# Kernel tuning notes

Hardware: AMD Instinct MI355X
Metric: run time of the kernel (lower is better)

The kernel has to match this reference:

```python
import jax, jax.numpy as jnp
import numpy as np

B, S, D, H = 4, 2048, 1024, 16
HD = D // H


def setup_inputs() -> dict:
    key = jax.random.key(0)
    ks = jax.random.split(key, 5)
    s_in = 1.0 / np.sqrt(D)
    return {
        "x": jax.random.normal(ks[0], (B, S, D), dtype=jnp.float32),
        "W_attn": jax.random.uniform(ks[1], (D, 3 * D), dtype=jnp.float32, minval=-s_in, maxval=s_in),
        "b_attn": jax.random.uniform(ks[2], (3 * D,), dtype=jnp.float32, minval=-s_in, maxval=s_in),
        "W_proj": jax.random.uniform(ks[3], (D, D), dtype=jnp.float32, minval=-s_in, maxval=s_in),
        "b_proj": jax.random.uniform(ks[4], (D,), dtype=jnp.float32, minval=-s_in, maxval=s_in),
    }


def reference(x, W_attn, b_attn, W_proj, b_proj):
    b, s, d = x.shape
    qkv = x @ W_attn + b_attn                      # [B,S,3D]
    q, k, v = jnp.split(qkv, 3, axis=-1)
    # [B,H,S,HD]
    q = q.reshape(b, s, H, HD).transpose(0, 2, 1, 3)
    k = k.reshape(b, s, H, HD).transpose(0, 2, 1, 3)
    v = v.reshape(b, s, H, HD).transpose(0, 2, 1, 3)
    scale = 1.0 / np.sqrt(HD)
    att = jnp.einsum("bhqd,bhkd->bhqk", q, k) * scale
    causal = jnp.tril(jnp.ones((s, s), dtype=bool))
    att = jnp.where(causal[None, None], att, -jnp.inf)
    att = jax.nn.softmax(att, axis=-1)
    y = jnp.einsum("bhqk,bhkd->bhqd", att, v)      # [B,H,S,HD]
    y = y.transpose(0, 2, 1, 3).reshape(b, s, d)
    return y @ W_proj + b_proj
```

## Files before the change

### kernel.cpp

```cpp
#include <hip/hip_runtime.h>

#define B_  4
#define S_  2048
#define D_  1024
#define H_  16
#define HD_ 64
#define BS_ (B_*S_)

typedef _Float16 f16;
typedef _Float16 f16_8 __attribute__((ext_vector_type(8)));
typedef _Float16 f16_4 __attribute__((ext_vector_type(4)));
typedef float    f32_4 __attribute__((ext_vector_type(4)));
typedef unsigned int u32;

#define MFMA32(a,b,c) __builtin_amdgcn_mfma_f32_16x16x32_f16(a, b, c, 0, 0, 0)
#define MFMA16(a,b,c) __builtin_amdgcn_mfma_f32_16x16x16f16(a, b, c, 0, 0, 0)
#define NEG_INF (-__builtin_inff())

__device__ inline void gl_lds16(const f16* g, f16* lds_base, int chunk_base) {
    __builtin_amdgcn_global_load_lds(
        (const __attribute__((address_space(1))) u32*)g,
        (__attribute__((address_space(3))) u32*)(lds_base + (size_t)chunk_base * 8),
        16, 0, 0);
}

__global__ __launch_bounds__(256) void prep(
    const float* __restrict__ X,  f16* __restrict__ Xh,
    const float* __restrict__ Wa, f16* __restrict__ Wta)
{
    __shared__ f16 T[64][72];
    const int t = threadIdx.x;
    const int bid = blockIdx.x;
    if (bid < 4096) {
        const size_t i = ((size_t)bid * 256 + t) * 8;
        float4 a = *(const float4*)&X[i];
        float4 b = *(const float4*)&X[i + 4];
        f16 h[8] = {(f16)a.x,(f16)a.y,(f16)a.z,(f16)a.w,
                    (f16)b.x,(f16)b.y,(f16)b.z,(f16)b.w};
        *(uint4*)&Xh[i] = *(const uint4*)h;
        return;
    }
    const int idx = bid - 4096;
    const int n0 = (idx % 48) * 64, k0 = (idx / 48) * 64;
    const int nl4 = (t & 15) * 4;
    #pragma unroll
    for (int r = 0; r < 4; r++) {
        const int kl = (t >> 4) + r * 16;
        float4 v = *(const float4*)&Wa[(size_t)(k0 + kl) * 3072 + n0 + nl4];
        T[nl4 + 0][kl] = (f16)v.x;
        T[nl4 + 1][kl] = (f16)v.y;
        T[nl4 + 2][kl] = (f16)v.z;
        T[nl4 + 3][kl] = (f16)v.w;
    }
    __syncthreads();
    const int nr = t >> 2, kc = (t & 3) * 16;
    *(uint4*)&Wta[(size_t)(n0 + nr) * 1024 + k0 + kc]     = *(uint4*)&T[nr][kc];
    *(uint4*)&Wta[(size_t)(n0 + nr) * 1024 + k0 + kc + 8] = *(uint4*)&T[nr][kc + 8];
}

__global__ __launch_bounds__(256) void trans_w(
    const float* __restrict__ W, f16* __restrict__ Wt, int ncols)
{
    __shared__ f16 T[64][72];
    const int t = threadIdx.x;
    const int n0 = blockIdx.x * 64, k0 = blockIdx.y * 64;
    const int nl4 = (t & 15) * 4;
    #pragma unroll
    for (int r = 0; r < 4; r++) {
        const int kl = (t >> 4) + r * 16;
        float4 v = *(const float4*)&W[(size_t)(k0 + kl) * ncols + n0 + nl4];
        T[nl4 + 0][kl] = (f16)v.x;
        T[nl4 + 1][kl] = (f16)v.y;
        T[nl4 + 2][kl] = (f16)v.z;
        T[nl4 + 3][kl] = (f16)v.w;
    }
    __syncthreads();
    const int nr = t >> 2, kc = (t & 3) * 16;
    *(uint4*)&Wt[(size_t)(n0 + nr) * 1024 + k0 + kc]     = *(uint4*)&T[nr][kc];
    *(uint4*)&Wt[(size_t)(n0 + nr) * 1024 + k0 + kc + 8] = *(uint4*)&T[nr][kc + 8];
}

__global__ __launch_bounds__(512, 2) void qkv_gemm(
    const f16*   __restrict__ Xh,
    const f16*   __restrict__ Wta,
    const float* __restrict__ bias,
    f16* __restrict__ Qb, f16* __restrict__ Kb, f16* __restrict__ Vt)
{
    __shared__ f16 lds[73728];

    const int t    = threadIdx.x;
    const int lane = t & 63;
    const int w    = t >> 6;
    const int quad = lane >> 4, l15 = lane & 15;
    const int wr = w >> 2, wc = w & 3;
    const int m0 = blockIdx.x * 128;
    const int n0 = blockIdx.y * 256;
    const int wb = t & 448;

    int aoff[2], boff[4];
    #pragma unroll
    for (int c = 0; c < 2; c++) {
        const int i = c*512 + t, row = i >> 3, sl = i & 7;
        aoff[c] = row*1024 + ((sl ^ (row & 7)) << 3);
    }
    #pragma unroll
    for (int c = 0; c < 4; c++) {
        const int i = c*512 + t, row = i >> 3, sl = i & 7;
        boff[c] = row*1024 + ((sl ^ (row & 7)) << 3);
    }
    int fa[4][2], fb[4][2];
    #pragma unroll
    for (int mi = 0; mi < 4; mi++)
        #pragma unroll
        for (int kk = 0; kk < 2; kk++)
            fa[mi][kk] = (wr*64 + mi*16 + l15)*64 + (((kk*4 + quad) ^ (l15 & 7)) << 3);
    #pragma unroll
    for (int ni = 0; ni < 4; ni++)
        #pragma unroll
        for (int kk = 0; kk < 2; kk++)
            fb[ni][kk] = (wc*64 + ni*16 + l15)*64 + (((kk*4 + quad) ^ (l15 & 7)) << 3);

    const f16* Ag = Xh  + (size_t)m0 * 1024;
    const f16* Bg = Wta + (size_t)n0 * 1024;

    f32_4 acc[4][4] = {};

    #pragma unroll
    for (int c = 0; c < 2; c++) gl_lds16(Ag + aoff[c],       lds,                c*512 + wb);
    #pragma unroll
    for (int c = 0; c < 4; c++) gl_lds16(Bg + boff[c],       lds + 8192,         c*512 + wb);
    #pragma unroll
    for (int c = 0; c < 2; c++) gl_lds16(Ag + 64 + aoff[c],  lds + 24576,        c*512 + wb);
    #pragma unroll
    for (int c = 0; c < 4; c++) gl_lds16(Bg + 64 + boff[c],  lds + 24576 + 8192, c*512 + wb);
    asm volatile("s_waitcnt vmcnt(6)" ::: "memory");
    __builtin_amdgcn_s_barrier();
    asm volatile("" ::: "memory");

    int cur = 0;
    #pragma unroll 1
    for (int T = 0; T < 16; T++) {
        f16* buf        = lds + cur*24576;
        const int nxt   = cur ? cur - 1 : 2;
        f16* nbuf       = lds + nxt*24576;
        const bool st   = (T < 14);
        const int  kt2  = (T + 2) * 64;

        if (st) {
            #pragma unroll
            for (int c = 0; c < 2; c++)
                gl_lds16(Ag + kt2 + aoff[c], nbuf, c*512 + wb);
        }
        f16_8 af[4][2], bf[2][2];
        #pragma unroll
        for (int mi = 0; mi < 4; mi++)
            #pragma unroll
            for (int kk = 0; kk < 2; kk++)
                af[mi][kk] = *(const f16_8*)&buf[fa[mi][kk]];
        #pragma unroll
        for (int ni = 0; ni < 2; ni++)
            #pragma unroll
            for (int kk = 0; kk < 2; kk++)
                bf[ni][kk] = *(const f16_8*)&buf[8192 + fb[ni][kk]];
        asm volatile("" ::: "memory");
        __builtin_amdgcn_s_barrier();
        asm volatile("" ::: "memory");
        __builtin_amdgcn_s_setprio(1);
        #pragma unroll
        for (int kk = 0; kk < 2; kk++)
            #pragma unroll
            for (int mi = 0; mi < 4; mi++)
                #pragma unroll
                for (int ni = 0; ni < 2; ni++)
                    acc[mi][ni] = MFMA32(af[mi][kk], bf[ni][kk], acc[mi][ni]);
        __builtin_amdgcn_s_setprio(0);
        asm volatile("" ::: "memory");
        __builtin_amdgcn_s_barrier();
        asm volatile("" ::: "memory");

        if (st) {
            #pragma unroll
            for (int c = 0; c < 4; c++)
                gl_lds16(Bg + kt2 + boff[c], nbuf + 8192, c*512 + wb);
        }
        #pragma unroll
        for (int ni = 0; ni < 2; ni++)
            #pragma unroll
            for (int kk = 0; kk < 2; kk++)
                bf[ni][kk] = *(const f16_8*)&buf[8192 + fb[2 + ni][kk]];
        asm volatile("" ::: "memory");
        __builtin_amdgcn_s_barrier();
        asm volatile("" ::: "memory");
        __builtin_amdgcn_s_setprio(1);
        #pragma unroll
        for (int kk = 0; kk < 2; kk++)
            #pragma unroll
            for (int mi = 0; mi < 4; mi++)
                #pragma unroll
                for (int ni = 0; ni < 2; ni++)
                    acc[mi][2 + ni] = MFMA32(af[mi][kk], bf[ni][kk], acc[mi][2 + ni]);
        __builtin_amdgcn_s_setprio(0);
        if (T < 14)       asm volatile("s_waitcnt vmcnt(6)" ::: "memory");
        else if (T == 14) asm volatile("s_waitcnt vmcnt(0)" ::: "memory");
        __builtin_amdgcn_s_barrier();
        asm volatile("" ::: "memory");

        cur = (cur >= 2) ? 0 : cur + 1;
    }

    const int which = n0 >> 10;
    float bcol[4];
    #pragma unroll
    for (int ni = 0; ni < 4; ni++)
        bcol[ni] = bias[n0 + wc*64 + ni*16 + l15];

    if (which < 2) {
        f16* dst = (which == 0) ? Qb : Kb;
        const float sc = (which == 0) ? 0.125f * 1.44269504f : 1.0f;
        #pragma unroll
        for (int mi = 0; mi < 4; mi++)
        #pragma unroll
        for (int ni = 0; ni < 4; ni++)
        #pragma unroll
        for (int r = 0; r < 4; r++) {
            int m = m0 + wr*64 + mi*16 + quad*4 + r;
            int n = (n0 & 1023) + wc*64 + ni*16 + l15;
            int h = n >> 6, hd = n & 63;
            int b = m >> 11, s = m & 2047;
            dst[((size_t)(b*16 + h)*2048 + s)*64 + hd] =
                (f16)((acc[mi][ni][r] + bcol[ni]) * sc);
        }
    } else {
        f16* Ct = lds;
        #pragma unroll
        for (int mi = 0; mi < 4; mi++)
        #pragma unroll
        for (int ni = 0; ni < 4; ni++)
        #pragma unroll
        for (int r = 0; r < 4; r++) {
            int nl = wc*64 + ni*16 + l15;
            int ml = wr*64 + mi*16 + quad*4 + r;
            Ct[nl*136 + ml] = (f16)(acc[mi][ni][r] + bcol[ni]);
        }
        __syncthreads();
        const int row = t >> 1, half = t & 1;
        const int nv = (n0 & 1023) + row;
        const int h = nv >> 6, hd = nv & 63;
        const int b = m0 >> 11;
        const int s0 = (m0 & 2047) + half*64;
        f16* dst = Vt + ((size_t)(b*16 + h)*64 + hd)*2048 + s0;
        #pragma unroll
        for (int j = 0; j < 8; j++)
            *(uint4*)&dst[j*8] = *(uint4*)&Ct[row*136 + half*64 + j*8];
    }
}

__global__ __launch_bounds__(256) void attn(
    const f16* __restrict__ Qb,
    const f16* __restrict__ Kb,
    const f16* __restrict__ Vt,
    f16* __restrict__ Y)
{
    __shared__ f16 Ks[64*72];
    __shared__ f16 Vs[64*72];

    const int t    = threadIdx.x;
    const int w    = t >> 6;
    const int lane = t & 63;
    const int quad = lane >> 4, l15 = lane & 15;
    const int bh   = blockIdx.x;
    const int b    = bh >> 4, h = bh & 15;

    const f16* qh = Qb + (size_t)bh * S_ * 64;
    const f16* kh = Kb + (size_t)bh * S_ * 64;
    const f16* vt = Vt + (size_t)bh * 64 * S_;

    const int sk = t >> 2, sc = (t & 3) * 8;
    const f16_4 ones = {(f16)1,(f16)1,(f16)1,(f16)1};

    #pragma unroll 1
    for (int sp = 0; sp < 2; sp++) {
        const int qb = sp ? 15 - (int)blockIdx.y : (int)blockIdx.y;
        const int qw = qb*128 + w*32;

        f16_8 qa[2][2];
        #pragma unroll
        for (int rt = 0; rt < 2; rt++)
            #pragma unroll
            for (int c = 0; c < 2; c++)
                qa[rt][c] = *(const f16_8*)&qh[(size_t)(qw + rt*16 + l15)*64 + c*32 + quad*8];

        f32_4 o[2][4] = {};
        f32_4 lacc[2] = {};
        const int ntiles = 2*qb + 2;

        for (int kt = 0; kt < ntiles; kt++) {
            const int kbase = kt * 64;
            *(uint4*)&Ks[sk*72 + sc]      = *(const uint4*)&kh[(size_t)(kbase + sk)*64 + sc];
            *(uint4*)&Ks[sk*72 + sc + 32] = *(const uint4*)&kh[(size_t)(kbase + sk)*64 + sc + 32];
            *(uint4*)&Vs[sk*72 + sc]      = *(const uint4*)&vt[(size_t)sk*2048 + kbase + sc];
            *(uint4*)&Vs[sk*72 + sc + 32] = *(const uint4*)&vt[(size_t)sk*2048 + kbase + sc + 32];
            __syncthreads();

            if (kbase <= qw + 31) {
                f16_8 kb[4][2];
                #pragma unroll
                for (int sub = 0; sub < 4; sub++)
                    #pragma unroll
                    for (int c = 0; c < 2; c++)
                        kb[sub][c] = *(const f16_8*)&Ks[(sub*16 + l15)*72 + c*32 + quad*8];
                f32_4 st[2][4];
                #pragma unroll
                for (int rt = 0; rt < 2; rt++)
                    #pragma unroll
                    for (int sub = 0; sub < 4; sub++) {
                        f32_4 a = {};
                        a = MFMA32(kb[sub][0], qa[rt][0], a);
                        a = MFMA32(kb[sub][1], qa[rt][1], a);
                        st[rt][sub] = a;
                    }

                const bool masked = (kbase + 63 > qw);
                f16_4 pt[2][4];
                #pragma unroll
                for (int rt = 0; rt < 2; rt++)
                #pragma unroll
                for (int sub = 0; sub < 4; sub++) {
                    const int qrow = qw + rt*16 + l15;
                    f16_4 p;
                    #pragma unroll
                    for (int r = 0; r < 4; r++) {
                        float x = st[rt][sub][r];
                        if (masked) {
                            int key = kbase + sub*16 + quad*4 + r;
                            x = (key <= qrow) ? x : NEG_INF;
                        }
                        p[r] = (f16)__builtin_amdgcn_exp2f(x);
                    }
                    pt[rt][sub] = p;
                }

                #pragma unroll
                for (int rt = 0; rt < 2; rt++) {
                    f16_4 ps = (pt[rt][0] + pt[rt][1]) + (pt[rt][2] + pt[rt][3]);
                    lacc[rt] = MFMA16(ps, ones, lacc[rt]);
                }

                #pragma unroll
                for (int sub = 0; sub < 4; sub++) {
                    f16_4 vb[4];
                    #pragma unroll
                    for (int tt = 0; tt < 4; tt++)
                        vb[tt] = *(const f16_4*)&Vs[(tt*16 + l15)*72 + sub*16 + quad*4];
                    #pragma unroll
                    for (int rt = 0; rt < 2; rt++)
                        #pragma unroll
                        for (int tt = 0; tt < 4; tt++)
                            o[rt][tt] = MFMA16(pt[rt][sub], vb[tt], o[rt][tt]);
                }
            }
            __syncthreads();
        }

        #pragma unroll
        for (int rt = 0; rt < 2; rt++)
        #pragma unroll
        for (int r = 0; r < 4; r++) {
            float inv = 1.0f / lacc[rt][r];
            int srow = qw + rt*16 + quad*4 + r;
            #pragma unroll
            for (int tt = 0; tt < 4; tt++)
                Y[(size_t)(b*S_ + srow)*1024 + h*64 + tt*16 + l15] =
                    (f16)(o[rt][tt][r] * inv);
        }
    }
}

__global__ __launch_bounds__(256) void proj_gemm(
    const f16* __restrict__ Yb,
    const f16* __restrict__ Wtp,
    const float* __restrict__ bias,
    float* __restrict__ Out)
{
    __shared__ f16 lds2[16384];
    f16* Af[2] = {lds2,        lds2 + 4096};
    f16* Bf[2] = {lds2 + 8192, lds2 + 12288};

    const int t    = threadIdx.x;
    const int lane = t & 63;
    const int w    = t >> 6;
    const int quad = lane >> 4, l15 = lane & 15;
    const int wr = w >> 1, wc = w & 1;
    const int m0 = blockIdx.x * 128;
    const int n0 = blockIdx.y * 128;
    const int wbase = t & 192;

    f32_4 acc[4][4] = {};

    for (int k0 = 0; k0 < 1024; k0 += 64) {
        #pragma unroll
        for (int kc = 0; kc < 2; kc++)
            #pragma unroll
            for (int c = 0; c < 2; c++) {
                int i = c*256 + t;
                const int row = i >> 2, col = (i & 3) * 8;
                gl_lds16(Yb  + (size_t)(m0 + row)*1024 + k0 + kc*32 + col,
                         Af[kc], c*256 + wbase);
                gl_lds16(Wtp + (size_t)(n0 + row)*1024 + k0 + kc*32 + col,
                         Bf[kc], c*256 + wbase);
            }
        __syncthreads();
        #pragma unroll
        for (int kc = 0; kc < 2; kc++) {
            f16_8 af[4], bf[4];
            #pragma unroll
            for (int mi = 0; mi < 4; mi++)
                af[mi] = *(const f16_8*)&Af[kc][(wr*64 + mi*16 + l15)*32 + quad*8];
            #pragma unroll
            for (int ni = 0; ni < 4; ni++)
                bf[ni] = *(const f16_8*)&Bf[kc][(wc*64 + ni*16 + l15)*32 + quad*8];
            #pragma unroll
            for (int mi = 0; mi < 4; mi++)
                #pragma unroll
                for (int ni = 0; ni < 4; ni++)
                    acc[mi][ni] = MFMA32(af[mi], bf[ni], acc[mi][ni]);
        }
        __syncthreads();
    }

    #pragma unroll
    for (int mi = 0; mi < 4; mi++)
    #pragma unroll
    for (int ni = 0; ni < 4; ni++)
    #pragma unroll
    for (int r = 0; r < 4; r++) {
        int m = m0 + wr*64 + mi*16 + quad*4 + r;
        int n = n0 + wc*64 + ni*16 + l15;
        Out[(size_t)m*1024 + n] = acc[mi][ni][r] + bias[n];
    }
}

extern "C" void kernel_launch(void* const* d_in, const int* in_sizes, int n_in,
                              void* d_out, int out_size, void* d_ws, size_t ws_size,
                              hipStream_t stream) {
    const float* x      = (const float*)d_in[0];
    const float* W_attn = (const float*)d_in[1];
    const float* b_attn = (const float*)d_in[2];
    const float* W_proj = (const float*)d_in[3];
    const float* b_proj = (const float*)d_in[4];
    float* out = (float*)d_out;

    const size_t per = (size_t)B_ * H_ * S_ * HD_;
    f16* Yb  = (f16*)d_ws;
    f16* Wta = Yb;
    f16* Qb  = Yb + per;
    f16* Kb  = Qb + per;
    f16* Vt  = Kb + per;
    f16* Wtp = Qb;
    f16* Xh  = (f16*)d_out;

    prep     <<<4096 + 768, 256, 0, stream>>>(x, Xh, W_attn, Wta);
    qkv_gemm <<<dim3(64, 12), 512, 0, stream>>>(Xh, Wta, b_attn, Qb, Kb, Vt);
    attn     <<<dim3(64, 8),  256, 0, stream>>>(Qb, Kb, Vt, Yb);
    trans_w  <<<dim3(16, 16), 256, 0, stream>>>(W_proj, Wtp, D_);
    proj_gemm<<<dim3(64, 8),  256, 0, stream>>>(Yb, Wtp, b_proj, out);
}
```

Baseline: 273.5 us.

## Restructure attention to 512 threads with double-buffered async K/V loads

The attention kernel now runs both paired query strips in one pass using 8 waves (512 threads) instead of looping over them sequentially. K/V tiles are loaded with global_load_lds into double-buffered, XOR-swizzled LDS, so the next tile's load overlaps compute on the current one, and raw s_barrier/waitcnt replace __syncthreads. MFMA sections get raised scheduling priority. This removes serialized load-then-compute stalls and LDS bank conflicts, at the cost of more LDS per block (64KB) and tighter register limits from launch_bounds(512,4).

```diff
diff --git a/kernel.cpp b/kernel.cpp
--- a/kernel.cpp
+++ b/kernel.cpp
@@ -255,14 +255,13 @@
     }
 }
 
-__global__ __launch_bounds__(256) void attn(
+__global__ __launch_bounds__(512, 4) void attn(
     const f16* __restrict__ Qb,
     const f16* __restrict__ Kb,
     const f16* __restrict__ Vt,
     f16* __restrict__ Y)
 {
-    __shared__ f16 Ks[64*72];
-    __shared__ f16 Vs[64*72];
+    __shared__ f16 lds[32768];
 
     const int t    = threadIdx.x;
     const int w    = t >> 6;
@@ -270,109 +269,131 @@
     const int quad = lane >> 4, l15 = lane & 15;
     const int bh   = blockIdx.x;
     const int b    = bh >> 4, h = bh & 15;
+    const int qbp  = blockIdx.y;
+    const int strip = (w < 4) ? qbp : 15 - qbp;
+    const int qw   = strip*128 + (w & 3)*32;
+    const int NT   = 32 - 2*qbp;
 
     const f16* qh = Qb + (size_t)bh * S_ * 64;
     const f16* kh = Kb + (size_t)bh * S_ * 64;
     const f16* vt = Vt + (size_t)bh * 64 * S_;
 
-    const int sk = t >> 2, sc = (t & 3) * 8;
+    const int srow = t >> 3;
+    const int sgk  = ((t & 7) ^ (srow & 7)) << 3;
+    const int wb   = t & 448;
+    const int l7   = l15 & 7;
     const f16_4 ones = {(f16)1,(f16)1,(f16)1,(f16)1};
 
+    f16_8 qa[2][2];
+    #pragma unroll
+    for (int rt = 0; rt < 2; rt++)
+        #pragma unroll
+        for (int c = 0; c < 2; c++)
+            qa[rt][c] = *(const f16_8*)&qh[(size_t)(qw + rt*16 + l15)*64 + c*32 + quad*8];
+
+    f32_4 o[2][4] = {};
+    f32_4 lacc[2] = {};
+
+    gl_lds16(kh + (size_t)srow*64 + sgk,  lds,        wb);
+    gl_lds16(vt + (size_t)srow*2048 + sgk, lds + 4096, wb);
+
     #pragma unroll 1
-    for (int sp = 0; sp < 2; sp++) {
-        const int qb = sp ? 15 - (int)blockIdx.y : (int)blockIdx.y;
-        const int qw = qb*128 + w*32;
-
-        f16_8 qa[2][2];
-        #pragma unroll
-        for (int rt = 0; rt < 2; rt++)
-            #pragma unroll
-            for (int c = 0; c < 2; c++)
-                qa[rt][c] = *(const f16_8*)&qh[(size_t)(qw + rt*16 + l15)*64 + c*32 + quad*8];
-
-        f32_4 o[2][4] = {};
-        f32_4 lacc[2] = {};
-        const int ntiles = 2*qb + 2;
-
-        for (int kt = 0; kt < ntiles; kt++) {
-            const int kbase = kt * 64;
-            *(uint4*)&Ks[sk*72 + sc]      = *(const uint4*)&kh[(size_t)(kbase + sk)*64 + sc];
-            *(uint4*)&Ks[sk*72 + sc + 32] = *(const uint4*)&kh[(size_t)(kbase + sk)*64 + sc + 32];
-            *(uint4*)&Vs[sk*72 + sc]      = *(const uint4*)&vt[(size_t)sk*2048 + kbase + sc];
-            *(uint4*)&Vs[sk*72 + sc + 32] = *(const uint4*)&vt[(size_t)sk*2048 + kbase + sc + 32];
-            __syncthreads();
-
-            if (kbase <= qw + 31) {
-                f16_8 kb[4][2];
-                #pragma unroll
-                for (int sub = 0; sub < 4; sub++)
-                    #pragma unroll
-                    for (int c = 0; c < 2; c++)
-                        kb[sub][c] = *(const f16_8*)&Ks[(sub*16 + l15)*72 + c*32 + quad*8];
-                f32_4 st[2][4];
+    for (int kt = 0; kt < NT; kt++) {
+        const int kbase = kt * 64;
+        f16* Ks = lds + (kt & 1) * 8192;
+        f16* Vs = Ks + 4096;
+
+        if (kt + 1 < NT) {
+            const int nb = kbase + 64;
+            f16* nK = lds + ((kt + 1) & 1) * 8192;
+            gl_lds16(kh + (size_t)(nb + srow)*64 + sgk, nK,        wb);
+            gl_lds16(vt + (size_t)srow*2048 + nb + sgk, nK + 4096, wb);
+            asm volatile("s_waitcnt vmcnt(2)" ::: "memory");
+        } else {
+            asm volatile("s_waitcnt vmcnt(0)" ::: "memory");
+        }
+        __builtin_amdgcn_s_barrier();
+        asm volatile("" ::: "memory");
+
+        if (kbase <= qw + 31) {
+            f16_8 kb[4][2];
+            #pragma unroll
+            for (int sub = 0; sub < 4; sub++)
+                #pragma unroll
+                for (int c = 0; c < 2; c++)
+                    kb[sub][c] = *(const f16_8*)
+                        &Ks[(sub*16 + l15)*64 + (((c*4 + quad) ^ l7) << 3)];
+            f32_4 st[2][4];
+            __builtin_amdgcn_s_setprio(1);
+            #pragma unroll
+            for (int rt = 0; rt < 2; rt++)
+                #pragma unroll
+                for (int sub = 0; sub < 4; sub++) {
+                    f32_4 a = {};
+                    a = MFMA32(kb[sub][0], qa[rt][0], a);
+                    a = MFMA32(kb[sub][1], qa[rt][1], a);
+                    st[rt][sub] = a;
+                }
+            __builtin_amdgcn_s_setprio(0);
+
+            const bool masked = (kbase + 63 > qw);
+            f16_4 pt[2][4];
+            #pragma unroll
+            for (int rt = 0; rt < 2; rt++)
+            #pragma unroll
+            for (int sub = 0; sub < 4; sub++) {
+                const int qrow = qw + rt*16 + l15;
+                f16_4 p;
+                #pragma unroll
+                for (int r = 0; r < 4; r++) {
+                    float x = st[rt][sub][r];
+                    if (masked) {
+                        int key = kbase + sub*16 + quad*4 + r;
+                        x = (key <= qrow) ? x : NEG_INF;
+                    }
+                    p[r] = (f16)__builtin_amdgcn_exp2f(x);
+                }
+                pt[rt][sub] = p;
+            }
+
+            #pragma unroll
+            for (int rt = 0; rt < 2; rt++) {
+                f16_4 ps = (pt[rt][0] + pt[rt][1]) + (pt[rt][2] + pt[rt][3]);
+                lacc[rt] = MFMA16(ps, ones, lacc[rt]);
+            }
+
+            __builtin_amdgcn_s_setprio(1);
+            #pragma unroll
+            for (int sub = 0; sub < 4; sub++) {
+                f16_4 vb[4];
+                #pragma unroll
+                for (int tt = 0; tt < 4; tt++)
+                    vb[tt] = *(const f16_4*)
+                        &Vs[(tt*16 + l15)*64 +
+                            ((((sub*2 + (quad >> 1)) ^ l7) << 3) + (quad & 1)*4)];
                 #pragma unroll
                 for (int rt = 0; rt < 2; rt++)
                     #pragma unroll
-                    for (int sub = 0; sub < 4; sub++) {
-                        f32_4 a = {};
-                        a = MFMA32(kb[sub][0], qa[rt][0], a);
-                        a = MFMA32(kb[sub][1], qa[rt][1], a);
-                        st[rt][sub] = a;
-                    }
-
-                const bool masked = (kbase + 63 > qw);
-                f16_4 pt[2][4];
-                #pragma unroll
-                for (int rt = 0; rt < 2; rt++)
-                #pragma unroll
-                for (int sub = 0; sub < 4; sub++) {
-                    const int qrow = qw + rt*16 + l15;
-                    f16_4 p;
-                    #pragma unroll
-                    for (int r = 0; r < 4; r++) {
-                        float x = st[rt][sub][r];
-                        if (masked) {
-                            int key = kbase + sub*16 + quad*4 + r;
-                            x = (key <= qrow) ? x : NEG_INF;
-                        }
-                        p[r] = (f16)__builtin_amdgcn_exp2f(x);
-                    }
-                    pt[rt][sub] = p;
-                }
-
-                #pragma unroll
-                for (int rt = 0; rt < 2; rt++) {
-                    f16_4 ps = (pt[rt][0] + pt[rt][1]) + (pt[rt][2] + pt[rt][3]);
-                    lacc[rt] = MFMA16(ps, ones, lacc[rt]);
-                }
-
-                #pragma unroll
-                for (int sub = 0; sub < 4; sub++) {
-                    f16_4 vb[4];
-                    #pragma unroll
                     for (int tt = 0; tt < 4; tt++)
-                        vb[tt] = *(const f16_4*)&Vs[(tt*16 + l15)*72 + sub*16 + quad*4];
-                    #pragma unroll
-                    for (int rt = 0; rt < 2; rt++)
-                        #pragma unroll
-                        for (int tt = 0; tt < 4; tt++)
-                            o[rt][tt] = MFMA16(pt[rt][sub], vb[tt], o[rt][tt]);
-                }
+                        o[rt][tt] = MFMA16(pt[rt][sub], vb[tt], o[rt][tt]);
             }
-            __syncthreads();
-        }
-
-        #pragma unroll
-        for (int rt = 0; rt < 2; rt++)
-        #pragma unroll
-        for (int r = 0; r < 4; r++) {
-            float inv = 1.0f / lacc[rt][r];
-            int srow = qw + rt*16 + quad*4 + r;
-            #pragma unroll
-            for (int tt = 0; tt < 4; tt++)
-                Y[(size_t)(b*S_ + srow)*1024 + h*64 + tt*16 + l15] =
-                    (f16)(o[rt][tt][r] * inv);
-        }
+            __builtin_amdgcn_s_setprio(0);
+        }
+        asm volatile("" ::: "memory");
+        __builtin_amdgcn_s_barrier();
+        asm volatile("" ::: "memory");
+    }
+
+    #pragma unroll
+    for (int rt = 0; rt < 2; rt++)
+    #pragma unroll
+    for (int r = 0; r < 4; r++) {
+        float inv = 1.0f / lacc[rt][r];
+        int srw = qw + rt*16 + quad*4 + r;
+        #pragma unroll
+        for (int tt = 0; tt < 4; tt++)
+            Y[(size_t)(b*S_ + srw)*1024 + h*64 + tt*16 + l15] =
+                (f16)(o[rt][tt][r] * inv);
     }
 }
 
@@ -461,7 +482,7 @@
 
     prep     <<<4096 + 768, 256, 0, stream>>>(x, Xh, W_attn, Wta);
     qkv_gemm <<<dim3(64, 12), 512, 0, stream>>>(Xh, Wta, b_attn, Qb, Kb, Vt);
-    attn     <<<dim3(64, 8),  256, 0, stream>>>(Qb, Kb, Vt, Yb);
+    attn     <<<dim3(64, 8),  512, 0, stream>>>(Qb, Kb, Vt, Yb);
     trans_w  <<<dim3(16, 16), 256, 0, stream>>>(W_proj, Wtp, D_);
     proj_gemm<<<dim3(64, 8),  256, 0, stream>>>(Yb, Wtp, b_proj, out);
 }
```

Measured after the change: 263.7 us. 3.6% less time.
